# Performance work log

Hardware: AMD Instinct MI355X
Metric: run time of the kernel (lower is better)

The kernel has to match this reference:

```python
import jax, jax.numpy as jnp
import numpy as np

N_HEAD = 12

def setup_inputs() -> dict:
    key = jax.random.key(0)
    k1, k2, k3 = jax.random.split(key, 3)
    B, T, C = 1, 4096, 768
    x = jax.random.normal(k1, (B, T, C), dtype=jnp.float32)
    w_attn = jax.random.normal(k2, (C, 3 * C), dtype=jnp.float32) * 0.02
    w_proj = jax.random.normal(k3, (C, C), dtype=jnp.float32) * 0.02
    return {"x": x, "w_attn": w_attn, "w_proj": w_proj}

def reference(x, w_attn, w_proj):
    B, T, C = x.shape
    H = N_HEAD
    hd = C // H
    scale = 1.0 / jnp.sqrt(jnp.asarray(hd, dtype=x.dtype))
    qkv = x @ w_attn  # [B,T,3C]
    q, k, v = jnp.split(qkv, 3, axis=-1)
    # [B,T,C] -> [B,H,T,hd]
    q = q.reshape(B, T, H, hd).transpose(0, 2, 1, 3)
    k = k.reshape(B, T, H, hd).transpose(0, 2, 1, 3)
    v = v.reshape(B, T, H, hd).transpose(0, 2, 1, 3)
    att = jnp.einsum("bhqd,bhkd->bhqk", q, k) * scale  # [B,H,T,T]
    causal = jnp.tril(jnp.ones((T, T), dtype=bool))
    att = jnp.where(causal[None, None], att, -jnp.inf)
    att = jax.nn.softmax(att, axis=-1)
    y = jnp.einsum("bhqk,bhkd->bhqd", att, v)  # [B,H,T,hd]
    y = y.transpose(0, 2, 1, 3).reshape(B, T, C)
    return y @ w_proj
```

## Files before the change

kernel.cpp:

```cpp
#include <hip/hip_runtime.h>
#include <hip/hip_bf16.h>

typedef __attribute__((ext_vector_type(8))) short bfx8;
typedef __attribute__((ext_vector_type(4))) short bfx4;
typedef __attribute__((ext_vector_type(4))) float f32x4;
typedef __attribute__((ext_vector_type(4))) unsigned int u32x4;
typedef __attribute__((ext_vector_type(2))) unsigned int u32x2;

#define T_SEQ 4096
#define C_DIM 768
#define NH    12
#define HD    64
#define QKV_N 2304
#define QK_N  1536

#define MFMA16(a, b, c) __builtin_amdgcn_mfma_f32_16x16x32_bf16((a), (b), (c), 0, 0, 0)

#if __has_builtin(__builtin_amdgcn_exp2f)
#define EXP2(x) __builtin_amdgcn_exp2f(x)
#else
#define EXP2(x) exp2f(x)
#endif

__device__ __forceinline__ short f2bf(float f) {
  __hip_bfloat16 h = __float2bfloat16(f);
  return __builtin_bit_cast(short, h);
}

__device__ __forceinline__ void pl16(unsigned& a, unsigned& b) {
#if __has_builtin(__builtin_amdgcn_permlane16_swap)
  u32x2 r = __builtin_amdgcn_permlane16_swap(a, b, false, false);
  a = r[0]; b = r[1];
#else
  unsigned ax = (unsigned)__shfl_xor((int)a, 16, 64);
  unsigned bx = (unsigned)__shfl_xor((int)b, 16, 64);
  bool odd = ((threadIdx.x >> 4) & 1) != 0;
  unsigned na = odd ? bx : a;
  unsigned nb = odd ? b : ax;
  a = na; b = nb;
#endif
}
__device__ __forceinline__ void pl32(unsigned& a, unsigned& b) {
#if __has_builtin(__builtin_amdgcn_permlane32_swap)
  u32x2 r = __builtin_amdgcn_permlane32_swap(a, b, false, false);
  a = r[0]; b = r[1];
#else
  unsigned ax = (unsigned)__shfl_xor((int)a, 32, 64);
  unsigned bx = (unsigned)__shfl_xor((int)b, 32, 64);
  bool hi = ((threadIdx.x >> 5) & 1) != 0;
  unsigned na = hi ? bx : a;
  unsigned nb = hi ? b : ax;
  a = na; b = nb;
#endif
}

#define NB_CONV 3072
#define NB_TA   (72 * 24)
#define NB_TB   (24 * 24)
__global__ __launch_bounds__(256) void prep_kernel(
    const float* __restrict__ x, short* __restrict__ xb,
    const float* __restrict__ w_attn, short* __restrict__ wab,
    const float* __restrict__ w_proj, short* __restrict__ wpb) {
  __shared__ short tile[32][33];
  const int b = blockIdx.x;
  if (b < NB_CONV) {
    int i = b * 256 + threadIdx.x;
    float4 v = ((const float4*)x)[i];
    bfx4 o;
    o[0] = f2bf(v.x); o[1] = f2bf(v.y); o[2] = f2bf(v.z); o[3] = f2bf(v.w);
    ((bfx4*)xb)[i] = o;
    return;
  }
  const float* in; short* out; int Cc, bx, by, qcols;
  if (b < NB_CONV + NB_TA) {
    int bb = b - NB_CONV;
    in = w_attn; out = wab; Cc = QKV_N;
    bx = (bb % 72) * 32; by = (bb / 72) * 32;
    qcols = C_DIM;
  } else {
    int bb = b - NB_CONV - NB_TA;
    in = w_proj; out = wpb; Cc = C_DIM;
    bx = (bb % 24) * 32; by = (bb / 24) * 32;
    qcols = 0;
  }
  int tx = threadIdx.x & 31, ty = threadIdx.x >> 5;
  float sc = (bx + tx) < qcols ? 0.125f * 1.4426950408889634f : 1.0f;
#pragma unroll
  for (int i = 0; i < 32; i += 8)
    tile[ty + i][tx] = f2bf(in[(size_t)(by + ty + i) * Cc + (bx + tx)] * sc);
  __syncthreads();
#pragma unroll
  for (int i = 0; i < 32; i += 8)
    out[(size_t)(bx + ty + i) * C_DIM + (by + tx)] = tile[tx][ty + i];
}

__global__ __launch_bounds__(256) void gemm_qkv(
    const short* __restrict__ A, const short* __restrict__ Bt,
    short* __restrict__ qk, short* __restrict__ Vt, int K) {
  __shared__ short As[2][128 * 32];
  __shared__ short Bs[2][128 * 32];
  const int tid  = threadIdx.x;
  const int lane = tid & 63;
  const int wave = tid >> 6;
  const int am0 = blockIdx.x * 128;
  const int bn0 = blockIdx.y * 128;
  const int wr = (wave >> 1) * 64;
  const int wc = (wave & 1) * 64;

  const int idx0 = tid,       r0 = idx0 >> 2, c0 = (idx0 & 3) * 8;
  const int idx1 = 256 + tid, r1 = idx1 >> 2, c1 = (idx1 & 3) * 8;

#define GSTAGE(buf, k0)                                                                 \
  do {                                                                                  \
    __builtin_amdgcn_global_load_lds(                                                   \
        (const __attribute__((address_space(1))) void*)(A + (size_t)(am0 + r0) * K + (k0) + c0), \
        (__attribute__((address_space(3))) void*)(&As[buf][idx0 * 8]), 16, 0, 0);       \
    __builtin_amdgcn_global_load_lds(                                                   \
        (const __attribute__((address_space(1))) void*)(A + (size_t)(am0 + r1) * K + (k0) + c1), \
        (__attribute__((address_space(3))) void*)(&As[buf][idx1 * 8]), 16, 0, 0);       \
    __builtin_amdgcn_global_load_lds(                                                   \
        (const __attribute__((address_space(1))) void*)(Bt + (size_t)(bn0 + r0) * K + (k0) + c0), \
        (__attribute__((address_space(3))) void*)(&Bs[buf][idx0 * 8]), 16, 0, 0);       \
    __builtin_amdgcn_global_load_lds(                                                   \
        (const __attribute__((address_space(1))) void*)(Bt + (size_t)(bn0 + r1) * K + (k0) + c1), \
        (__attribute__((address_space(3))) void*)(&Bs[buf][idx1 * 8]), 16, 0, 0);       \
  } while (0)

  const f32x4 zero = {0.f, 0.f, 0.f, 0.f};
  f32x4 acc[4][4];
#pragma unroll
  for (int i = 0; i < 4; i++)
#pragma unroll
    for (int j = 0; j < 4; j++) acc[i][j] = zero;

  const int aoff = (wr + (lane & 15)) * 32 + (lane >> 4) * 8;
  const int boff = (wc + (lane & 15)) * 32 + (lane >> 4) * 8;

  const int nk = K / 32;
  GSTAGE(0, 0);
  for (int t = 0; t < nk; t++) {
    const int cur = t & 1;
    if (t + 1 < nk) {
      GSTAGE(cur ^ 1, (t + 1) * 32);
      asm volatile("s_waitcnt vmcnt(4)" ::: "memory");
    } else {
      asm volatile("s_waitcnt vmcnt(0)" ::: "memory");
    }
    __builtin_amdgcn_s_barrier();

    bfx8 a[4], b[4];
#pragma unroll
    for (int mf = 0; mf < 4; mf++)
      a[mf] = *(const bfx8*)&As[cur][aoff + mf * 16 * 32];
#pragma unroll
    for (int nf = 0; nf < 4; nf++)
      b[nf] = *(const bfx8*)&Bs[cur][boff + nf * 16 * 32];
#pragma unroll
    for (int mf = 0; mf < 4; mf++)
#pragma unroll
      for (int nf = 0; nf < 4; nf++)
        acc[mf][nf] = MFMA16(a[mf], b[nf], acc[mf][nf]);

    asm volatile("s_waitcnt lgkmcnt(0)" ::: "memory");
    __builtin_amdgcn_s_barrier();
  }
#undef GSTAGE

  if (bn0 >= QK_N) {
#pragma unroll
    for (int mf = 0; mf < 4; mf++) {
      int row0 = am0 + wr + mf * 16 + (lane >> 4) * 4;
#pragma unroll
      for (int nf = 0; nf < 4; nf++) {
        int colV = bn0 - QK_N + wc + nf * 16 + (lane & 15);
        bfx4 ov;
#pragma unroll
        for (int r = 0; r < 4; r++) ov[r] = f2bf(acc[mf][nf][r]);
        *(bfx4*)&Vt[(size_t)colV * T_SEQ + row0] = ov;
      }
    }
  } else {
#pragma unroll
    for (int mf = 0; mf < 4; mf++) {
#pragma unroll
      for (int r = 0; r < 4; r++) {
        int row = am0 + wr + mf * 16 + (lane >> 4) * 4 + r;
#pragma unroll
        for (int nf = 0; nf < 4; nf++) {
          int col = bn0 + wc + nf * 16 + (lane & 15);
          qk[(size_t)row * QK_N + col] = f2bf(acc[mf][nf][r]);
        }
      }
    }
  }
}

__global__ __launch_bounds__(256) void gemm_proj(
    const short* __restrict__ A, const short* __restrict__ Bt,
    float* __restrict__ C, int N, int K) {
  __shared__ short As[2][64 * 32];
  __shared__ short Bs[2][64 * 32];
  const int tid  = threadIdx.x;
  const int lane = tid & 63;
  const int wave = tid >> 6;
  const int am0 = blockIdx.x * 64;
  const int bn0 = blockIdx.y * 64;
  const int wr = (wave >> 1) * 32;
  const int wc = (wave & 1) * 32;

  const int r0 = tid >> 2, c0 = (tid & 3) * 8;

#define PSTAGE(buf, k0)                                                                 \
  do {                                                                                  \
    __builtin_amdgcn_global_load_lds(                                                   \
        (const __attribute__((address_space(1))) void*)(A + (size_t)(am0 + r0) * K + (k0) + c0), \
        (__attribute__((address_space(3))) void*)(&As[buf][tid * 8]), 16, 0, 0);        \
    __builtin_amdgcn_global_load_lds(                                                   \
        (const __attribute__((address_space(1))) void*)(Bt + (size_t)(bn0 + r0) * K + (k0) + c0), \
        (__attribute__((address_space(3))) void*)(&Bs[buf][tid * 8]), 16, 0, 0);        \
  } while (0)

  const f32x4 zero = {0.f, 0.f, 0.f, 0.f};
  f32x4 acc[2][2];
#pragma unroll
  for (int i = 0; i < 2; i++)
#pragma unroll
    for (int j = 0; j < 2; j++) acc[i][j] = zero;

  const int aoff = (wr + (lane & 15)) * 32 + (lane >> 4) * 8;
  const int boff = (wc + (lane & 15)) * 32 + (lane >> 4) * 8;

  const int nk = K / 32;
  PSTAGE(0, 0);
  for (int t = 0; t < nk; t++) {
    const int cur = t & 1;
    if (t + 1 < nk) {
      PSTAGE(cur ^ 1, (t + 1) * 32);
      asm volatile("s_waitcnt vmcnt(2)" ::: "memory");
    } else {
      asm volatile("s_waitcnt vmcnt(0)" ::: "memory");
    }
    __builtin_amdgcn_s_barrier();

    bfx8 a[2], b[2];
#pragma unroll
    for (int mf = 0; mf < 2; mf++)
      a[mf] = *(const bfx8*)&As[cur][aoff + mf * 16 * 32];
#pragma unroll
    for (int nf = 0; nf < 2; nf++)
      b[nf] = *(const bfx8*)&Bs[cur][boff + nf * 16 * 32];
#pragma unroll
    for (int mf = 0; mf < 2; mf++)
#pragma unroll
      for (int nf = 0; nf < 2; nf++)
        acc[mf][nf] = MFMA16(a[mf], b[nf], acc[mf][nf]);

    asm volatile("s_waitcnt lgkmcnt(0)" ::: "memory");
    __builtin_amdgcn_s_barrier();
  }
#undef PSTAGE

#pragma unroll
  for (int mf = 0; mf < 2; mf++) {
#pragma unroll
    for (int r = 0; r < 4; r++) {
      int row = am0 + wr + mf * 16 + (lane >> 4) * 4 + r;
#pragma unroll
      for (int nf = 0; nf < 2; nf++) {
        int col = bn0 + wc + nf * 16 + (lane & 15);
        C[(size_t)row * N + col] = acc[mf][nf][r];
      }
    }
  }
}

__global__ __launch_bounds__(256) void attn_kernel(
    const short* __restrict__ qk, const short* __restrict__ Vt,
    short* __restrict__ yb) {
  __shared__ short Ks[2][64 * 64];
  __shared__ short Vs[2][64 * 64];

  const int tid  = threadIdx.x;
  const int lane = tid & 63;
  const int wv   = tid >> 6;
  const int col  = lane & 15;
  const int g    = lane >> 4;

  const int bid = blockIdx.x;
  const int h   = bid % NH;
  const int pr  = bid / NH;
  const int myi = (wv < 2) ? (127 - pr) : pr;
  const int qw  = myi * 32 + (wv & 1) * 16;
  const int nt  = ((127 - pr) * 32 + 31) / 64 + 1;

  const int hq = h * HD;
  const int hk = C_DIM + h * HD;
  const short* Vth = Vt + (size_t)h * HD * T_SEQ;

  const int sidx0 = tid;
  const int sidx1 = 256 + tid;
  const int srow0 = sidx0 >> 3, sslot0 = (sidx0 & 7) ^ (srow0 & 7);
  const int srow1 = sidx1 >> 3, sslot1 = (sidx1 & 7) ^ (srow1 & 7);

#define STAGE(buf, kvoff)                                                               \
  do {                                                                                  \
    __builtin_amdgcn_global_load_lds(                                                   \
        (const __attribute__((address_space(1))) void*)(qk + (size_t)((kvoff) + srow0) * QK_N + hk + sslot0 * 8), \
        (__attribute__((address_space(3))) void*)(&Ks[buf][sidx0 * 8]), 16, 0, 0);      \
    __builtin_amdgcn_global_load_lds(                                                   \
        (const __attribute__((address_space(1))) void*)(qk + (size_t)((kvoff) + srow1) * QK_N + hk + sslot1 * 8), \
        (__attribute__((address_space(3))) void*)(&Ks[buf][sidx1 * 8]), 16, 0, 0);      \
    __builtin_amdgcn_global_load_lds(                                                   \
        (const __attribute__((address_space(1))) void*)(Vth + (size_t)srow0 * T_SEQ + (kvoff) + sslot0 * 8), \
        (__attribute__((address_space(3))) void*)(&Vs[buf][sidx0 * 8]), 16, 0, 0);      \
    __builtin_amdgcn_global_load_lds(                                                   \
        (const __attribute__((address_space(1))) void*)(Vth + (size_t)srow1 * T_SEQ + (kvoff) + sslot1 * 8), \
        (__attribute__((address_space(3))) void*)(&Vs[buf][sidx1 * 8]), 16, 0, 0);      \
  } while (0)

  bfx8 qf[2];
#pragma unroll
  for (int hf = 0; hf < 2; hf++)
    qf[hf] = *(const bfx8*)&qk[(size_t)(qw + col) * QK_N + hq + hf * 32 + g * 8];

  int koff[4][2], voff[2][4];
#pragma unroll
  for (int sub = 0; sub < 4; sub++) {
    int row = sub * 16 + col;
#pragma unroll
    for (int hf = 0; hf < 2; hf++)
      koff[sub][hf] = row * 64 + ((((hf << 2) | g) ^ (row & 7)) * 8);
  }
#pragma unroll
  for (int ks = 0; ks < 2; ks++)
#pragma unroll
    for (int c = 0; c < 4; c++) {
      int row = c * 16 + col;
      voff[ks][c] = row * 64 + ((((ks << 2) | g) ^ (row & 7)) * 8);
    }

  bfx8 ones;
#pragma unroll
  for (int j = 0; j < 8; j++) ones[j] = (short)0x3F80;

  const f32x4 zero = {0.f, 0.f, 0.f, 0.f};
  f32x4 o[4];
#pragma unroll
  for (int c = 0; c < 4; c++) o[c] = zero;
  f32x4 o_l = zero;

  const int qabs = qw + col;

#define TILE_BODY(BUF, KV)                                                              \
  do {                                                                                  \
    if ((KV) <= qw + 15) {                                                              \
      bfx8 kf[4][2];                                                                    \
      _Pragma("unroll") for (int sub = 0; sub < 4; sub++)                               \
          _Pragma("unroll") for (int hf = 0; hf < 2; hf++)                              \
              kf[sub][hf] = *(const bfx8*)&Ks[BUF][koff[sub][hf]];                      \
      bfx8 vtf[2][4];                                                                   \
      _Pragma("unroll") for (int ks = 0; ks < 2; ks++)                                  \
          _Pragma("unroll") for (int c = 0; c < 4; c++)                                 \
              vtf[ks][c] = *(const bfx8*)&Vs[BUF][voff[ks][c]];                         \
      f32x4 s[4];                                                                       \
      __builtin_amdgcn_s_setprio(1);                                                    \
      _Pragma("unroll") for (int sub = 0; sub < 4; sub++) {                             \
        s[sub] = zero;                                                                  \
        s[sub] = MFMA16(kf[sub][0], qf[0], s[sub]);                                     \
        s[sub] = MFMA16(kf[sub][1], qf[1], s[sub]);                                     \
      }                                                                                 \
      __builtin_amdgcn_s_setprio(0);                                                    \
      if (!((KV) + 63 <= qw)) {                                                         \
        _Pragma("unroll") for (int sub = 0; sub < 4; sub++)                             \
            _Pragma("unroll") for (int r = 0; r < 4; r++) {                             \
              int key = (KV) + sub * 16 + 4 * g + r;                                    \
              if (key > qabs) s[sub][r] = -INFINITY;                                    \
            }                                                                           \
      }                                                                                 \
      unsigned u[4][4];                                                                 \
      _Pragma("unroll") for (int sub = 0; sub < 4; sub++)                               \
          _Pragma("unroll") for (int r = 0; r < 4; r++) {                               \
            float pv = EXP2(s[sub][r]);                                                 \
            u[sub][r] = __builtin_bit_cast(unsigned, pv) & 0xFFFF0000u;                 \
          }                                                                             \
      _Pragma("unroll") for (int ks = 0; ks < 2; ks++) {                                \
        unsigned x0 = u[2 * ks][1] | (u[2 * ks][0] >> 16);                              \
        unsigned y0 = u[2 * ks + 1][1] | (u[2 * ks + 1][0] >> 16);                      \
        unsigned x1 = u[2 * ks][3] | (u[2 * ks][2] >> 16);                              \
        unsigned y1 = u[2 * ks + 1][3] | (u[2 * ks + 1][2] >> 16);                      \
        pl32(x0, y0); pl16(x0, y0);                                                     \
        pl32(x1, y1); pl16(x1, y1);                                                     \
        u32x4 w; w[0] = x0; w[1] = x1; w[2] = y0; w[3] = y1;                            \
        bfx8 pf = __builtin_bit_cast(bfx8, w);                                          \
        __builtin_amdgcn_s_setprio(1);                                                  \
        _Pragma("unroll") for (int c = 0; c < 4; c++)                                   \
            o[c] = MFMA16(vtf[ks][c], pf, o[c]);                                        \
        o_l = MFMA16(ones, pf, o_l);                                                    \
        __builtin_amdgcn_s_setprio(0);                                                  \
      }                                                                                 \
    }                                                                                   \
  } while (0)

  STAGE(0, 0);

  int t = 0;
  while (true) {
    if (t + 1 < nt) {
      STAGE(1, (t + 1) * 64);
      asm volatile("s_waitcnt vmcnt(4)" ::: "memory");
    } else {
      asm volatile("s_waitcnt vmcnt(0)" ::: "memory");
    }
    __builtin_amdgcn_s_barrier();
    TILE_BODY(0, t * 64);
    asm volatile("s_waitcnt lgkmcnt(0)" ::: "memory");
    __builtin_amdgcn_s_barrier();
    if (++t >= nt) break;

    if (t + 1 < nt) {
      STAGE(0, (t + 1) * 64);
      asm volatile("s_waitcnt vmcnt(4)" ::: "memory");
    } else {
      asm volatile("s_waitcnt vmcnt(0)" ::: "memory");
    }
    __builtin_amdgcn_s_barrier();
    TILE_BODY(1, t * 64);
    asm volatile("s_waitcnt lgkmcnt(0)" ::: "memory");
    __builtin_amdgcn_s_barrier();
    if (++t >= nt) break;
  }

  float inv = 1.f / o_l[0];
#pragma unroll
  for (int c = 0; c < 4; c++) {
    bfx4 ov;
#pragma unroll
    for (int r = 0; r < 4; r++) ov[r] = f2bf(o[c][r] * inv);
    *(bfx4*)&yb[(size_t)(qw + col) * C_DIM + h * HD + c * 16 + g * 4] = ov;
  }
#undef TILE_BODY
#undef STAGE
}

extern "C" void kernel_launch(void* const* d_in, const int* in_sizes, int n_in,
                              void* d_out, int out_size, void* d_ws, size_t ws_size,
                              hipStream_t stream) {
  const float* x      = (const float*)d_in[0];
  const float* w_attn = (const float*)d_in[1];
  const float* w_proj = (const float*)d_in[2];
  float* out = (float*)d_out;

  char* ws = (char*)d_ws;
  short* xb  = (short*)(ws);
  short* wab = (short*)(ws + 6291456);
  short* wpb = (short*)(ws + 9830400);
  short* qk  = (short*)(ws + 11010048);
  short* Vt  = (short*)(ws + 23592960);
  short* yb  = (short*)(ws + 29884416);

  prep_kernel<<<NB_CONV + NB_TA + NB_TB, 256, 0, stream>>>(x, xb, w_attn, wab, w_proj, wpb);
  gemm_qkv<<<dim3(T_SEQ / 128, QKV_N / 128), 256, 0, stream>>>(xb, wab, qk, Vt, C_DIM);
  attn_kernel<<<64 * NH, 256, 0, stream>>>(qk, Vt, yb);
  gemm_proj<<<dim3(T_SEQ / 64, C_DIM / 64), 256, 0, stream>>>(yb, wpb, out, C_DIM, C_DIM);
}
```

Baseline: 112.6 us.

## Triple-buffer LDS pipelines in GEMMs and attention, drop second barrier per tile

Moves the QKV GEMM, projection GEMM and attention kernels from double-buffered to triple-buffered LDS staging. Each kernel now prefetches two tiles ahead and issues the next load after a single barrier per iteration, removing the trailing barrier. In attention, the bf16 truncating pack of probabilities becomes a single byte-permute instruction. LDS use grows by half, which may reduce occupancy, and the vmcnt wait counts now have to match the deeper prefetch.

```diff
diff --git a/kernel.cpp b/kernel.cpp
--- a/kernel.cpp
+++ b/kernel.cpp
@@ -25,6 +25,16 @@
 __device__ __forceinline__ short f2bf(float f) {
   __hip_bfloat16 h = __float2bfloat16(f);
   return __builtin_bit_cast(short, h);
+}
+
+__device__ __forceinline__ unsigned packtrunc(float p_even, float p_odd) {
+#if __has_builtin(__builtin_amdgcn_perm)
+  return __builtin_amdgcn_perm(__builtin_bit_cast(unsigned, p_odd),
+                               __builtin_bit_cast(unsigned, p_even), 0x07060302u);
+#else
+  return (__builtin_bit_cast(unsigned, p_odd) & 0xFFFF0000u) |
+         (__builtin_bit_cast(unsigned, p_even) >> 16);
+#endif
 }
 
 __device__ __forceinline__ void pl16(unsigned& a, unsigned& b) {
@@ -97,8 +107,8 @@
 __global__ __launch_bounds__(256) void gemm_qkv(
     const short* __restrict__ A, const short* __restrict__ Bt,
     short* __restrict__ qk, short* __restrict__ Vt, int K) {
-  __shared__ short As[2][128 * 32];
-  __shared__ short Bs[2][128 * 32];
+  __shared__ short As[3][128 * 32];
+  __shared__ short Bs[3][128 * 32];
   const int tid  = threadIdx.x;
   const int lane = tid & 63;
   const int wave = tid >> 6;
@@ -136,34 +146,39 @@
   const int aoff = (wr + (lane & 15)) * 32 + (lane >> 4) * 8;
   const int boff = (wc + (lane & 15)) * 32 + (lane >> 4) * 8;
 
+#define GBODY(BUF)                                                                      \
+  do {                                                                                  \
+    bfx8 a[4], b[4];                                                                    \
+    _Pragma("unroll") for (int mf = 0; mf < 4; mf++)                                    \
+        a[mf] = *(const bfx8*)&As[BUF][aoff + mf * 16 * 32];                            \
+    _Pragma("unroll") for (int nf = 0; nf < 4; nf++)                                    \
+        b[nf] = *(const bfx8*)&Bs[BUF][boff + nf * 16 * 32];                            \
+    _Pragma("unroll") for (int mf = 0; mf < 4; mf++)                                    \
+        _Pragma("unroll") for (int nf = 0; nf < 4; nf++)                                \
+            acc[mf][nf] = MFMA16(a[mf], b[nf], acc[mf][nf]);                            \
+  } while (0)
+
+#define GPHASE(BCUR, BNXT2)                                                             \
+  do {                                                                                  \
+    if (t + 1 < nk) { asm volatile("s_waitcnt vmcnt(4)" ::: "memory"); }                \
+    else            { asm volatile("s_waitcnt vmcnt(0)" ::: "memory"); }                \
+    __builtin_amdgcn_s_barrier();                                                       \
+    if (t + 2 < nk) GSTAGE(BNXT2, (t + 2) * 32);                                        \
+    GBODY(BCUR);                                                                        \
+    asm volatile("s_waitcnt lgkmcnt(0)" ::: "memory");                                  \
+  } while (0)
+
   const int nk = K / 32;
   GSTAGE(0, 0);
-  for (int t = 0; t < nk; t++) {
-    const int cur = t & 1;
-    if (t + 1 < nk) {
-      GSTAGE(cur ^ 1, (t + 1) * 32);
-      asm volatile("s_waitcnt vmcnt(4)" ::: "memory");
-    } else {
-      asm volatile("s_waitcnt vmcnt(0)" ::: "memory");
-    }
-    __builtin_amdgcn_s_barrier();
-
-    bfx8 a[4], b[4];
-#pragma unroll
-    for (int mf = 0; mf < 4; mf++)
-      a[mf] = *(const bfx8*)&As[cur][aoff + mf * 16 * 32];
-#pragma unroll
-    for (int nf = 0; nf < 4; nf++)
-      b[nf] = *(const bfx8*)&Bs[cur][boff + nf * 16 * 32];
-#pragma unroll
-    for (int mf = 0; mf < 4; mf++)
-#pragma unroll
-      for (int nf = 0; nf < 4; nf++)
-        acc[mf][nf] = MFMA16(a[mf], b[nf], acc[mf][nf]);
-
-    asm volatile("s_waitcnt lgkmcnt(0)" ::: "memory");
-    __builtin_amdgcn_s_barrier();
-  }
+  GSTAGE(1, 32);
+  int t = 0;
+  while (true) {
+    GPHASE(0, 2); if (++t >= nk) break;
+    GPHASE(1, 0); if (++t >= nk) break;
+    GPHASE(2, 1); if (++t >= nk) break;
+  }
+#undef GPHASE
+#undef GBODY
 #undef GSTAGE
 
   if (bn0 >= QK_N) {
@@ -198,8 +213,8 @@
 __global__ __launch_bounds__(256) void gemm_proj(
     const short* __restrict__ A, const short* __restrict__ Bt,
     float* __restrict__ C, int N, int K) {
-  __shared__ short As[2][64 * 32];
-  __shared__ short Bs[2][64 * 32];
+  __shared__ short As[3][64 * 32];
+  __shared__ short Bs[3][64 * 32];
   const int tid  = threadIdx.x;
   const int lane = tid & 63;
   const int wave = tid >> 6;
@@ -230,34 +245,39 @@
   const int aoff = (wr + (lane & 15)) * 32 + (lane >> 4) * 8;
   const int boff = (wc + (lane & 15)) * 32 + (lane >> 4) * 8;
 
+#define PBODY(BUF)                                                                      \
+  do {                                                                                  \
+    bfx8 a[2], b[2];                                                                    \
+    _Pragma("unroll") for (int mf = 0; mf < 2; mf++)                                    \
+        a[mf] = *(const bfx8*)&As[BUF][aoff + mf * 16 * 32];                            \
+    _Pragma("unroll") for (int nf = 0; nf < 2; nf++)                                    \
+        b[nf] = *(const bfx8*)&Bs[BUF][boff + nf * 16 * 32];                            \
+    _Pragma("unroll") for (int mf = 0; mf < 2; mf++)                                    \
+        _Pragma("unroll") for (int nf = 0; nf < 2; nf++)                                \
+            acc[mf][nf] = MFMA16(a[mf], b[nf], acc[mf][nf]);                            \
+  } while (0)
+
+#define PPHASE(BCUR, BNXT2)                                                             \
+  do {                                                                                  \
+    if (t + 1 < nk) { asm volatile("s_waitcnt vmcnt(2)" ::: "memory"); }                \
+    else            { asm volatile("s_waitcnt vmcnt(0)" ::: "memory"); }                \
+    __builtin_amdgcn_s_barrier();                                                       \
+    if (t + 2 < nk) PSTAGE(BNXT2, (t + 2) * 32);                                        \
+    PBODY(BCUR);                                                                        \
+    asm volatile("s_waitcnt lgkmcnt(0)" ::: "memory");                                  \
+  } while (0)
+
   const int nk = K / 32;
   PSTAGE(0, 0);
-  for (int t = 0; t < nk; t++) {
-    const int cur = t & 1;
-    if (t + 1 < nk) {
-      PSTAGE(cur ^ 1, (t + 1) * 32);
-      asm volatile("s_waitcnt vmcnt(2)" ::: "memory");
-    } else {
-      asm volatile("s_waitcnt vmcnt(0)" ::: "memory");
-    }
-    __builtin_amdgcn_s_barrier();
-
-    bfx8 a[2], b[2];
-#pragma unroll
-    for (int mf = 0; mf < 2; mf++)
-      a[mf] = *(const bfx8*)&As[cur][aoff + mf * 16 * 32];
-#pragma unroll
-    for (int nf = 0; nf < 2; nf++)
-      b[nf] = *(const bfx8*)&Bs[cur][boff + nf * 16 * 32];
-#pragma unroll
-    for (int mf = 0; mf < 2; mf++)
-#pragma unroll
-      for (int nf = 0; nf < 2; nf++)
-        acc[mf][nf] = MFMA16(a[mf], b[nf], acc[mf][nf]);
-
-    asm volatile("s_waitcnt lgkmcnt(0)" ::: "memory");
-    __builtin_amdgcn_s_barrier();
-  }
+  PSTAGE(1, 32);
+  int t = 0;
+  while (true) {
+    PPHASE(0, 2); if (++t >= nk) break;
+    PPHASE(1, 0); if (++t >= nk) break;
+    PPHASE(2, 1); if (++t >= nk) break;
+  }
+#undef PPHASE
+#undef PBODY
 #undef PSTAGE
 
 #pragma unroll
@@ -277,8 +297,8 @@
 __global__ __launch_bounds__(256) void attn_kernel(
     const short* __restrict__ qk, const short* __restrict__ Vt,
     short* __restrict__ yb) {
-  __shared__ short Ks[2][64 * 64];
-  __shared__ short Vs[2][64 * 64];
+  __shared__ short Ks[3][64 * 64];
+  __shared__ short Vs[3][64 * 64];
 
   const int tid  = threadIdx.x;
   const int lane = tid & 63;
@@ -377,17 +397,15 @@
               if (key > qabs) s[sub][r] = -INFINITY;                                    \
             }                                                                           \
       }                                                                                 \
-      unsigned u[4][4];                                                                 \
+      float p[4][4];                                                                    \
       _Pragma("unroll") for (int sub = 0; sub < 4; sub++)                               \
-          _Pragma("unroll") for (int r = 0; r < 4; r++) {                               \
-            float pv = EXP2(s[sub][r]);                                                 \
-            u[sub][r] = __builtin_bit_cast(unsigned, pv) & 0xFFFF0000u;                 \
-          }                                                                             \
+          _Pragma("unroll") for (int r = 0; r < 4; r++)                                 \
+              p[sub][r] = EXP2(s[sub][r]);                                              \
       _Pragma("unroll") for (int ks = 0; ks < 2; ks++) {                                \
-        unsigned x0 = u[2 * ks][1] | (u[2 * ks][0] >> 16);                              \
-        unsigned y0 = u[2 * ks + 1][1] | (u[2 * ks + 1][0] >> 16);                      \
-        unsigned x1 = u[2 * ks][3] | (u[2 * ks][2] >> 16);                              \
-        unsigned y1 = u[2 * ks + 1][3] | (u[2 * ks + 1][2] >> 16);                      \
+        unsigned x0 = packtrunc(p[2 * ks][0], p[2 * ks][1]);                            \
+        unsigned y0 = packtrunc(p[2 * ks + 1][0], p[2 * ks + 1][1]);                    \
+        unsigned x1 = packtrunc(p[2 * ks][2], p[2 * ks][3]);                            \
+        unsigned y1 = packtrunc(p[2 * ks + 1][2], p[2 * ks + 1][3]);                    \
         pl32(x0, y0); pl16(x0, y0);                                                     \
         pl32(x1, y1); pl16(x1, y1);                                                     \
         u32x4 w; w[0] = x0; w[1] = x1; w[2] = y0; w[3] = y1;                            \
@@ -401,33 +419,24 @@
     }                                                                                   \
   } while (0)
 
+#define PHASE(BCUR, BNXT2)                                                              \
+  do {                                                                                  \
+    if (t + 1 < nt) { asm volatile("s_waitcnt vmcnt(4)" ::: "memory"); }                \
+    else            { asm volatile("s_waitcnt vmcnt(0)" ::: "memory"); }                \
+    __builtin_amdgcn_s_barrier();                                                       \
+    if (t + 2 < nt) STAGE(BNXT2, (t + 2) * 64);                                         \
+    TILE_BODY(BCUR, t * 64);                                                            \
+    asm volatile("s_waitcnt lgkmcnt(0)" ::: "memory");                                  \
+  } while (0)
+
   STAGE(0, 0);
+  STAGE(1, 64);
 
   int t = 0;
   while (true) {
-    if (t + 1 < nt) {
-      STAGE(1, (t + 1) * 64);
-      asm volatile("s_waitcnt vmcnt(4)" ::: "memory");
-    } else {
-      asm volatile("s_waitcnt vmcnt(0)" ::: "memory");
-    }
-    __builtin_amdgcn_s_barrier();
-    TILE_BODY(0, t * 64);
-    asm volatile("s_waitcnt lgkmcnt(0)" ::: "memory");
-    __builtin_amdgcn_s_barrier();
-    if (++t >= nt) break;
-
-    if (t + 1 < nt) {
-      STAGE(0, (t + 1) * 64);
-      asm volatile("s_waitcnt vmcnt(4)" ::: "memory");
-    } else {
-      asm volatile("s_waitcnt vmcnt(0)" ::: "memory");
-    }
-    __builtin_amdgcn_s_barrier();
-    TILE_BODY(1, t * 64);
-    asm volatile("s_waitcnt lgkmcnt(0)" ::: "memory");
-    __builtin_amdgcn_s_barrier();
-    if (++t >= nt) break;
+    PHASE(0, 2); if (++t >= nt) break;
+    PHASE(1, 0); if (++t >= nt) break;
+    PHASE(2, 1); if (++t >= nt) break;
   }
 
   float inv = 1.f / o_l[0];
@@ -438,6 +447,7 @@
     for (int r = 0; r < 4; r++) ov[r] = f2bf(o[c][r] * inv);
     *(bfx4*)&yb[(size_t)(qw + col) * C_DIM + h * HD + c * 16 + g * 4] = ov;
   }
+#undef PHASE
 #undef TILE_BODY
 #undef STAGE
 }
```

New measurement: 121.0 us. 1.07x slower.

## Triple-buffer K/V tiles with one barrier per tile and v_perm bf16 packing

Applied to the files above, without the earlier changes.

The attention kernel moves from a double-buffered K/V pipeline with two barriers per tile to a triple-buffered one. Tile t+2 is staged after a single barrier, and loads run two tiles ahead. The exp-to-bf16 truncation and packing now use a single v_perm byte permute instead of separate mask, shift and or operations. In exchange, LDS use grows by half (48 KB per block), which may lower occupancy. The vmcnt(4) accounting now has to cover two outstanding stages, which could leave the wait on the current tile incorrect.

```diff
diff --git a/kernel.cpp b/kernel.cpp
--- a/kernel.cpp
+++ b/kernel.cpp
@@ -25,6 +25,16 @@
 __device__ __forceinline__ short f2bf(float f) {
   __hip_bfloat16 h = __float2bfloat16(f);
   return __builtin_bit_cast(short, h);
+}
+
+__device__ __forceinline__ unsigned packtrunc(float p_even, float p_odd) {
+#if __has_builtin(__builtin_amdgcn_perm)
+  return __builtin_amdgcn_perm(__builtin_bit_cast(unsigned, p_odd),
+                               __builtin_bit_cast(unsigned, p_even), 0x07060302u);
+#else
+  return (__builtin_bit_cast(unsigned, p_odd) & 0xFFFF0000u) |
+         (__builtin_bit_cast(unsigned, p_even) >> 16);
+#endif
 }
 
 __device__ __forceinline__ void pl16(unsigned& a, unsigned& b) {
@@ -277,8 +287,8 @@
 __global__ __launch_bounds__(256) void attn_kernel(
     const short* __restrict__ qk, const short* __restrict__ Vt,
     short* __restrict__ yb) {
-  __shared__ short Ks[2][64 * 64];
-  __shared__ short Vs[2][64 * 64];
+  __shared__ short Ks[3][64 * 64];
+  __shared__ short Vs[3][64 * 64];
 
   const int tid  = threadIdx.x;
   const int lane = tid & 63;
@@ -377,17 +387,15 @@
               if (key > qabs) s[sub][r] = -INFINITY;                                    \
             }                                                                           \
       }                                                                                 \
-      unsigned u[4][4];                                                                 \
+      float p[4][4];                                                                    \
       _Pragma("unroll") for (int sub = 0; sub < 4; sub++)                               \
-          _Pragma("unroll") for (int r = 0; r < 4; r++) {                               \
-            float pv = EXP2(s[sub][r]);                                                 \
-            u[sub][r] = __builtin_bit_cast(unsigned, pv) & 0xFFFF0000u;                 \
-          }                                                                             \
+          _Pragma("unroll") for (int r = 0; r < 4; r++)                                 \
+              p[sub][r] = EXP2(s[sub][r]);                                              \
       _Pragma("unroll") for (int ks = 0; ks < 2; ks++) {                                \
-        unsigned x0 = u[2 * ks][1] | (u[2 * ks][0] >> 16);                              \
-        unsigned y0 = u[2 * ks + 1][1] | (u[2 * ks + 1][0] >> 16);                      \
-        unsigned x1 = u[2 * ks][3] | (u[2 * ks][2] >> 16);                              \
-        unsigned y1 = u[2 * ks + 1][3] | (u[2 * ks + 1][2] >> 16);                      \
+        unsigned x0 = packtrunc(p[2 * ks][0], p[2 * ks][1]);                            \
+        unsigned y0 = packtrunc(p[2 * ks + 1][0], p[2 * ks + 1][1]);                    \
+        unsigned x1 = packtrunc(p[2 * ks][2], p[2 * ks][3]);                            \
+        unsigned y1 = packtrunc(p[2 * ks + 1][2], p[2 * ks + 1][3]);                    \
         pl32(x0, y0); pl16(x0, y0);                                                     \
         pl32(x1, y1); pl16(x1, y1);                                                     \
         u32x4 w; w[0] = x0; w[1] = x1; w[2] = y0; w[3] = y1;                            \
@@ -401,33 +409,24 @@
     }                                                                                   \
   } while (0)
 
+#define PHASE(BCUR, BNXT2)                                                              \
+  do {                                                                                  \
+    if (t + 1 < nt) { asm volatile("s_waitcnt vmcnt(4)" ::: "memory"); }                \
+    else            { asm volatile("s_waitcnt vmcnt(0)" ::: "memory"); }                \
+    __builtin_amdgcn_s_barrier();                                                       \
+    if (t + 2 < nt) STAGE(BNXT2, (t + 2) * 64);                                         \
+    TILE_BODY(BCUR, t * 64);                                                            \
+    asm volatile("s_waitcnt lgkmcnt(0)" ::: "memory");                                  \
+  } while (0)
+
   STAGE(0, 0);
+  STAGE(1, 64);
 
   int t = 0;
   while (true) {
-    if (t + 1 < nt) {
-      STAGE(1, (t + 1) * 64);
-      asm volatile("s_waitcnt vmcnt(4)" ::: "memory");
-    } else {
-      asm volatile("s_waitcnt vmcnt(0)" ::: "memory");
-    }
-    __builtin_amdgcn_s_barrier();
-    TILE_BODY(0, t * 64);
-    asm volatile("s_waitcnt lgkmcnt(0)" ::: "memory");
-    __builtin_amdgcn_s_barrier();
-    if (++t >= nt) break;
-
-    if (t + 1 < nt) {
-      STAGE(0, (t + 1) * 64);
-      asm volatile("s_waitcnt vmcnt(4)" ::: "memory");
-    } else {
-      asm volatile("s_waitcnt vmcnt(0)" ::: "memory");
-    }
-    __builtin_amdgcn_s_barrier();
-    TILE_BODY(1, t * 64);
-    asm volatile("s_waitcnt lgkmcnt(0)" ::: "memory");
-    __builtin_amdgcn_s_barrier();
-    if (++t >= nt) break;
+    PHASE(0, 2); if (++t >= nt) break;
+    PHASE(1, 0); if (++t >= nt) break;
+    PHASE(2, 1); if (++t >= nt) break;
   }
 
   float inv = 1.f / o_l[0];
@@ -438,6 +437,7 @@
     for (int r = 0; r < 4; r++) ov[r] = f2bf(o[c][r] * inv);
     *(bfx4*)&yb[(size_t)(qw + col) * C_DIM + h * HD + c * 16 + g * 4] = ov;
   }
+#undef PHASE
 #undef TILE_BODY
 #undef STAGE
 }
```

New measurement: 105.4 us. -6.4%, faster.
